# Optimization experiments

Measured on AMD Instinct MI355X. Metric: run time of the kernel, lower is better.

The kernel has to match this reference:

```python
import jax, jax.numpy as jnp
import numpy as np

DIM = 256
DT_REF = 1.0
EPS = 1e-7
GATE_MIN, GATE_MAX = 0.01, 0.99


def _safe_forcing(exp_arg):
    # expm1(z)/z with denominator regularized by sign of real part (matches torch _safe_forcing)
    safe_denom = exp_arg + EPS * jnp.sign(exp_arg.real + EPS)
    return (jnp.exp(exp_arg) - 1.0) / safe_denom


def setup_inputs() -> dict:
    key = jax.random.key(0)
    ks = jax.random.split(key, 12)
    B, T, D = 8, 4096, DIM
    x_mean_seq = jax.random.normal(ks[0], (B, T, D), dtype=jnp.float32)
    dt_seq = jax.random.uniform(ks[1], (B, T), dtype=jnp.float32)
    # GlobalFluxTracker params
    decay_re = jax.random.normal(ks[2], (D,), dtype=jnp.float32) * 0.1 - 1.0
    decay_im = jax.random.normal(ks[3], (D,), dtype=jnp.float32) * 0.1
    W_in = jax.random.normal(ks[4], (2 * D, 2 * D), dtype=jnp.float32) * (1.0 / np.sqrt(2 * D))
    b_in = jnp.zeros((2 * D,), dtype=jnp.float32)
    W_out = jax.random.normal(ks[5], (2 * D, 2 * D), dtype=jnp.float32) * (1.0 / np.sqrt(2 * D))
    b_out = jnp.zeros((2 * D,), dtype=jnp.float32)
    W_gate = jax.random.normal(ks[6], (D, 2 * D), dtype=jnp.float32) * (1.0 / np.sqrt(2 * D))
    b_gate = jnp.zeros((D,), dtype=jnp.float32)
    # TemporalPropagator diagonal generator params
    lam_re = jax.random.normal(ks[7], (D,), dtype=jnp.float32) * 0.01
    lam_im = jax.random.normal(ks[8], (D,), dtype=jnp.float32) * 0.1
    return {
        "x_mean_seq": x_mean_seq, "dt_seq": dt_seq,
        "decay_re": decay_re, "decay_im": decay_im,
        "W_in": W_in, "b_in": b_in, "W_out": W_out, "b_out": b_out,
        "W_gate": W_gate, "b_gate": b_gate,
        "lam_re": lam_re, "lam_im": lam_im,
    }


def reference(x_mean_seq, dt_seq, decay_re, decay_im, W_in, b_in,
              W_out, b_out, W_gate, b_gate, lam_re, lam_im):
    # dt ratio [B,T,1]
    dt_ratio = (dt_seq / DT_REF)[..., None]

    # --- GlobalFluxTracker.get_scan_operators ---
    lam_f = -jax.nn.softplus(decay_re) + 1j * decay_im          # [D] complex64
    exp_arg = lam_f[None, None, :] * dt_ratio                    # [B,T,D]
    decay = jnp.exp(exp_arg)                                     # [B,T,D]
    forcing = _safe_forcing(exp_arg)                             # [B,T,D]

    # _mix_input on real input (imag part is zero)
    x_cat = jnp.concatenate([x_mean_seq, jnp.zeros_like(x_mean_seq)], axis=-1)
    x_in = x_cat @ W_in.T + b_in                                 # [B,T,2D]
    x_re, x_im = jnp.split(x_in, 2, axis=-1)
    x_mixed = x_re + 1j * x_im                                   # [B,T,D]
    X_scan = x_mixed * forcing                                   # [B,T,D]

    # --- linear recurrence flux_t = decay_t * flux_{t-1} + X_t (associative scan over T) ---
    def combine(c1, c2):
        a1, b1 = c1
        a2, b2 = c2
        return (a1 * a2, b1 * a2 + b2)
    _, flux = jax.lax.associative_scan(combine, (decay, X_scan), axis=1)  # [B,T,D]

    # --- compute_output_seq ---
    s_cat = jnp.concatenate([flux.real, flux.imag], axis=-1)     # [B,T,2D]
    src = s_cat @ W_out.T + b_out
    src_re, src_im = jnp.split(src, 2, axis=-1)
    gate = jax.nn.sigmoid(s_cat @ W_gate.T + b_gate)
    gate = gate * (GATE_MAX - GATE_MIN) + GATE_MIN               # [B,T,D]

    # --- TemporalPropagator.get_transition_operators_seq ---
    lam_p = -jax.nn.softplus(lam_re) + 1j * lam_im
    exp_arg_p = lam_p[None, None, :] * dt_ratio
    decay_p = jnp.exp(exp_arg_p)
    forcing_p = _safe_forcing(exp_arg_p)

    out = jnp.concatenate([
        src_re, src_im, gate,
        decay_p.real, decay_p.imag, forcing_p.real, forcing_p.imag,
    ], axis=-1)                                                  # [B,T,7D]
    return out
```

## Files before the change

kernel.cpp:

```cpp
#include <hip/hip_runtime.h>
#include <math.h>

#define DD 256
#define TT 4096
#define NBATCH 8
#define BTOK 32768
#define EPSF 1e-7f

typedef __attribute__((ext_vector_type(4))) float f32x4;
typedef __attribute__((ext_vector_type(8))) short bf16x8;

__device__ __forceinline__ float softplusf(float x) {
  float e = __expf(-fabsf(x));
  return fmaxf(x, 0.f) + __logf(1.f + e);
}
__device__ __forceinline__ float bf2f(unsigned short u) {
  union { unsigned int i; float f; } v; v.i = ((unsigned int)u) << 16; return v.f;
}
__device__ __forceinline__ unsigned short f2bf(float f) {
  union { float f; unsigned int i; } v; v.f = f;
  unsigned int x = v.i;
  unsigned int lsb = (x >> 16) & 1u;
  x += 0x7fffu + lsb;
  return (unsigned short)(x >> 16);
}
__device__ __forceinline__ void decay_forcing(float are, float aim,
    float& dre, float& dim, float& fre, float& fim) {
  float e = __expf(are);
  float s = __sinf(aim), c = __cosf(aim);
  dre = e * c; dim = e * s;
  float sg = (are + EPSF >= 0.f) ? 1.f : -1.f;
  float denr = are + EPSF * sg;
  float deni = aim;
  float inv = __builtin_amdgcn_rcpf(denr * denr + deni * deni);
  float nr = dre - 1.f, ni = dim;
  fre = (nr * denr + ni * deni) * inv;
  fim = (ni * denr - nr * deni) * inv;
}
__device__ __forceinline__ void gl_lds16(const void* g, void* l) {
  __builtin_amdgcn_global_load_lds(
      (const __attribute__((address_space(1))) unsigned int*)g,
      (__attribute__((address_space(3))) unsigned int*)l, 16, 0, 0);
}

__global__ __launch_bounds__(256) void prep(
    const float* __restrict__ x, unsigned short* __restrict__ Xb,
    const float* __restrict__ Win, unsigned short* __restrict__ Wp1)
{
  const int bid = blockIdx.x;
  if (bid < 8192) {
    size_t i = ((size_t)bid * 256 + threadIdx.x) * 4;
    float4 v = *reinterpret_cast<const float4*>(&x[i]);
    ushort4 u;
    u.x = f2bf(v.x); u.y = f2bf(v.y); u.z = f2bf(v.z); u.w = f2bf(v.w);
    *reinterpret_cast<ushort4*>(&Xb[i]) = u;
  } else {
    const int p = bid - 8192;
    const int k = threadIdx.x;
    const int g = p >> 5, r = p & 31;
    const int src = (r < 16) ? (g * 16 + r) : (256 + g * 16 + (r - 16));
    Wp1[(size_t)p * 256 + k] = f2bf(Win[(size_t)src * 512 + k]);
  }
}

__global__ __launch_bounds__(256) void k1_mfma(
    const unsigned short* __restrict__ Xb,
    const unsigned short* __restrict__ Wp,
    const float* __restrict__ bin, const float* __restrict__ dts,
    const float* __restrict__ decr, const float* __restrict__ deci,
    unsigned int* __restrict__ Xri)
{
  __shared__ __align__(16) unsigned short As[128 * 64];
  __shared__ __align__(16) unsigned short Bs[128 * 64];
  const int bx = blockIdx.x;
  const int wg = (bx & 7) * 128 + (bx >> 3);
  const int mt = wg >> 2, nt = wg & 3;
  const int m0 = mt * 128, n0 = nt * 128;
  const int tid = threadIdx.x;
  const int lane = tid & 63, wid = tid >> 6;
  const int wr = wid >> 1, wc = wid & 1;
  const int l15 = lane & 15, hi = lane >> 4;
  const int lrow = tid >> 3;
  const int sslot = (tid & 7) ^ (lrow & 7);
  f32x4 acc[4][4];
  f32x4 z = {0.f, 0.f, 0.f, 0.f};
#pragma unroll
  for (int i = 0; i < 4; ++i)
#pragma unroll
    for (int j = 0; j < 4; ++j) acc[i][j] = z;

  for (int k0 = 0; k0 < 256; k0 += 64) {
    __syncthreads();
#pragma unroll
    for (int c = 0; c < 4; ++c) {
      gl_lds16(&Xb[(size_t)(m0 + c * 32 + lrow) * 256 + k0 + sslot * 8],
               &As[c * 2048 + tid * 8]);
      gl_lds16(&Wp[(size_t)(n0 + c * 32 + lrow) * 256 + k0 + sslot * 8],
               &Bs[c * 2048 + tid * 8]);
    }
    __syncthreads();
#pragma unroll
    for (int kk = 0; kk < 2; ++kk) {
      bf16x8 af[4], bfr[4];
      const int rslot = ((kk * 4 + hi) ^ (l15 & 7)) * 8;
#pragma unroll
      for (int m = 0; m < 4; ++m)
        af[m] = *reinterpret_cast<const bf16x8*>(&As[(wr * 64 + m * 16 + l15) * 64 + rslot]);
#pragma unroll
      for (int n = 0; n < 4; ++n)
        bfr[n] = *reinterpret_cast<const bf16x8*>(&Bs[(wc * 64 + n * 16 + l15) * 64 + rslot]);
#pragma unroll
      for (int m = 0; m < 4; ++m)
#pragma unroll
        for (int n = 0; n < 4; ++n)
          acc[m][n] = __builtin_amdgcn_mfma_f32_16x16x32_bf16(af[m], bfr[n], acc[m][n], 0, 0, 0);
    }
  }

  const int pbase = n0 + wc * 64;
#pragma unroll
  for (int pr = 0; pr < 2; ++pr) {
    const int d = (pbase >> 1) + pr * 16 + l15;
    const float nre = -softplusf(decr[d]);
    const float di = deci[d];
    const float br = bin[d], bi = bin[d + 256];
#pragma unroll
    for (int m = 0; m < 4; ++m) {
#pragma unroll
      for (int r = 0; r < 4; ++r) {
        const int row = m0 + wr * 64 + m * 16 + hi * 4 + r;
        float xr = acc[m][2 * pr][r] + br;
        float xi = acc[m][2 * pr + 1][r] + bi;
        float dt = dts[row];
        float are = nre * dt, aim = di * dt;
        float dr_, dm_, fr_, fm_;
        decay_forcing(are, aim, dr_, dm_, fr_, fm_);
        unsigned int pk = (unsigned int)f2bf(xr * fr_ - xi * fm_)
                        | ((unsigned int)f2bf(xr * fm_ + xi * fr_) << 16);
        Xri[(size_t)row * DD + d] = pk;
      }
    }
  }
}

__global__ __launch_bounds__(256) void k2a_wp3(
    const unsigned int* __restrict__ Xri,
    const float* __restrict__ dts, const float* __restrict__ decr,
    const float* __restrict__ deci,
    float4* __restrict__ ops,
    const float* __restrict__ Wout, const float* __restrict__ Wgate,
    unsigned short* __restrict__ Wp3)
{
  const int bx = blockIdx.x;
  if (bx >= 512) {
    const int p = bx - 512;
    const float* src = (p < 512) ? (Wout + (size_t)p * 512)
                                 : (Wgate + (size_t)(p - 512) * 512);
    Wp3[(size_t)p * 512 + threadIdx.x] = f2bf(src[threadIdx.x]);
    Wp3[(size_t)p * 512 + threadIdx.x + 256] = f2bf(src[threadIdx.x + 256]);
    return;
  }
  const int b = bx >> 6, c = bx & 63;
  const int d = threadIdx.x;
  __shared__ float sdt[64];
  if (threadIdx.x < 64) sdt[threadIdx.x] = dts[b * TT + c * 64 + threadIdx.x];
  const float nre = -softplusf(decr[d]);
  const float di = deci[d];
  __syncthreads();
  float Ar = 1.f, Ai = 0.f, Br = 0.f, Bi = 0.f;
  size_t base = (size_t)(b * TT + c * 64) * DD + d;
  for (int i = 0; i < 64; ++i) {
    float dt = sdt[i];
    float e = __expf(nre * dt);
    float s = __sinf(di * dt), cs = __cosf(di * dt);
    float ar = e * cs, ai = e * s;
    unsigned int pk = Xri[base]; base += DD;
    float xr = bf2f((unsigned short)(pk & 0xffffu));
    float xi = bf2f((unsigned short)(pk >> 16));
    float nAr = Ar * ar - Ai * ai, nAi = Ar * ai + Ai * ar;
    Ar = nAr; Ai = nAi;
    float nBr = Br * ar - Bi * ai + xr, nBi = Br * ai + Bi * ar + xi;
    Br = nBr; Bi = nBi;
  }
  ops[(size_t)bx * DD + d] = make_float4(Ar, Ai, Br, Bi);
}

__global__ __launch_bounds__(256) void k2c_apply(
    const unsigned int* __restrict__ Xri,
    const float* __restrict__ dts, const float* __restrict__ decr,
    const float* __restrict__ deci,
    const float4* __restrict__ ops,
    unsigned short* __restrict__ F)
{
  const int bx = blockIdx.x;
  const int b = bx >> 6, c = bx & 63;
  const int d = threadIdx.x;
  __shared__ float sdt[64];
  if (threadIdx.x < 64) sdt[threadIdx.x] = dts[b * TT + c * 64 + threadIdx.x];
  const float nre = -softplusf(decr[d]);
  const float di = deci[d];
  __syncthreads();

  float hr = 0.f, hi2 = 0.f;
  const size_t obase = (size_t)(b * 64) * DD + d;
  for (int c0 = 0; c0 < c; c0 += 8) {
    float4 oo[8];
#pragma unroll
    for (int j = 0; j < 8; ++j)
      oo[j] = (c0 + j < c) ? ops[obase + (size_t)(c0 + j) * DD]
                           : make_float4(1.f, 0.f, 0.f, 0.f);
#pragma unroll
    for (int j = 0; j < 8; ++j) {
      float nr = oo[j].x * hr - oo[j].y * hi2 + oo[j].z;
      float ni = oo[j].x * hi2 + oo[j].y * hr + oo[j].w;
      hr = nr; hi2 = ni;
    }
  }

  const int tok0 = b * TT + c * 64;
  size_t base = (size_t)tok0 * DD + d;
  for (int i = 0; i < 64; ++i) {
    float dt = sdt[i];
    float e = __expf(nre * dt);
    float s = __sinf(di * dt), cs = __cosf(di * dt);
    float ar = e * cs, ai = e * s;
    unsigned int pk = Xri[base]; base += DD;
    float xr = bf2f((unsigned short)(pk & 0xffffu));
    float xi = bf2f((unsigned short)(pk >> 16));
    float nr = ar * hr - ai * hi2 + xr;
    float ni = ar * hi2 + ai * hr + xi;
    hr = nr; hi2 = ni;
    size_t fb = (size_t)(tok0 + i) * 512 + d;
    F[fb] = f2bf(hr);
    F[fb + 256] = f2bf(hi2);
  }
}

__global__ __launch_bounds__(256) void k3k4(
    const unsigned short* __restrict__ F,
    const unsigned short* __restrict__ Wp,
    const float* __restrict__ bout, const float* __restrict__ bgate,
    const float* __restrict__ dts, const float* __restrict__ lre,
    const float* __restrict__ lim,
    float* __restrict__ out)
{
  __shared__ __align__(16) unsigned short As[128 * 64];
  __shared__ __align__(16) unsigned short Bs[128 * 64];

  const int q = blockIdx.x / 5, r5 = blockIdx.x % 5;

  if (r5 >= 3) {
    const int pb = q * 2 + (r5 - 3);
    const int d = threadIdx.x;
    const float nl = -softplusf(lre[d]);
    const float li = lim[d];
    const int tok0 = pb * 32;
#pragma unroll 4
    for (int i = 0; i < 32; ++i) {
      const int tok = tok0 + i;
      float dt = dts[tok];
      float dr, dm, fr, fm;
      decay_forcing(nl * dt, li * dt, dr, dm, fr, fm);
      float* o = out + (size_t)tok * 1792 + 768;
      __builtin_nontemporal_store(dr, &o[d]);
      __builtin_nontemporal_store(dm, &o[256 + d]);
      __builtin_nontemporal_store(fr, &o[512 + d]);
      __builtin_nontemporal_store(fm, &o[768 + d]);
    }
    return;
  }

  const int gw = q * 3 + r5;
  const int wg = (gw & 7) * 192 + (gw >> 3);
  const int mt = wg / 6, nt = wg % 6;
  const int m0 = mt * 128, n0 = nt * 128;
  const int tid = threadIdx.x;
  const int lane = tid & 63, wid = tid >> 6;
  const int wr = wid >> 1, wc = wid & 1;
  const int l15 = lane & 15, hi = lane >> 4;
  const int lrow = tid >> 3;
  const int sslot = (tid & 7) ^ (lrow & 7);
  f32x4 acc[4][4];
  f32x4 z = {0.f, 0.f, 0.f, 0.f};
#pragma unroll
  for (int i = 0; i < 4; ++i)
#pragma unroll
    for (int j = 0; j < 4; ++j) acc[i][j] = z;

  for (int k0 = 0; k0 < 512; k0 += 64) {
    __syncthreads();
#pragma unroll
    for (int c = 0; c < 4; ++c) {
      gl_lds16(&F[(size_t)(m0 + c * 32 + lrow) * 512 + k0 + sslot * 8],
               &As[c * 2048 + tid * 8]);
      gl_lds16(&Wp[(size_t)(n0 + c * 32 + lrow) * 512 + k0 + sslot * 8],
               &Bs[c * 2048 + tid * 8]);
    }
    __syncthreads();
    __builtin_amdgcn_s_setprio(1);
#pragma unroll
    for (int kk = 0; kk < 2; ++kk) {
      bf16x8 af[4], bfr[4];
      const int rslot = ((kk * 4 + hi) ^ (l15 & 7)) * 8;
#pragma unroll
      for (int m = 0; m < 4; ++m)
        af[m] = *reinterpret_cast<const bf16x8*>(&As[(wr * 64 + m * 16 + l15) * 64 + rslot]);
#pragma unroll
      for (int n = 0; n < 4; ++n)
        bfr[n] = *reinterpret_cast<const bf16x8*>(&Bs[(wc * 64 + n * 16 + l15) * 64 + rslot]);
#pragma unroll
      for (int m = 0; m < 4; ++m)
#pragma unroll
        for (int n = 0; n < 4; ++n)
          acc[m][n] = __builtin_amdgcn_mfma_f32_16x16x32_bf16(af[m], bfr[n], acc[m][n], 0, 0, 0);
    }
    __builtin_amdgcn_s_setprio(0);
  }

  const int nb = n0 + wc * 64;
  if (nb < 512) {
#pragma unroll
    for (int j = 0; j < 4; ++j) {
      const int col = nb + j * 16 + l15;
      const float bb = bout[col];
#pragma unroll
      for (int m = 0; m < 4; ++m)
#pragma unroll
        for (int r = 0; r < 4; ++r) {
          const int row = m0 + wr * 64 + m * 16 + hi * 4 + r;
          __builtin_nontemporal_store(acc[m][j][r] + bb, &out[(size_t)row * 1792 + col]);
        }
    }
  } else {
#pragma unroll
    for (int j = 0; j < 4; ++j) {
      const int col = nb + j * 16 + l15;
      const float bb = bgate[col - 512];
#pragma unroll
      for (int m = 0; m < 4; ++m)
#pragma unroll
        for (int r = 0; r < 4; ++r) {
          const int row = m0 + wr * 64 + m * 16 + hi * 4 + r;
          float g = __builtin_amdgcn_rcpf(1.f + __expf(-(acc[m][j][r] + bb)));
          __builtin_nontemporal_store(g * 0.98f + 0.01f, &out[(size_t)row * 1792 + col]);
        }
    }
  }
}

extern "C" void kernel_launch(void* const* d_in, const int* in_sizes, int n_in,
                              void* d_out, int out_size, void* d_ws, size_t ws_size,
                              hipStream_t stream)
{
  const float* x     = (const float*)d_in[0];
  const float* dts   = (const float*)d_in[1];
  const float* decr  = (const float*)d_in[2];
  const float* deci  = (const float*)d_in[3];
  const float* Win   = (const float*)d_in[4];
  const float* bin   = (const float*)d_in[5];
  const float* Wout  = (const float*)d_in[6];
  const float* bout  = (const float*)d_in[7];
  const float* Wgate = (const float*)d_in[8];
  const float* bgate = (const float*)d_in[9];
  const float* lre   = (const float*)d_in[10];
  const float* lim   = (const float*)d_in[11];
  float* out = (float*)d_out;
  char* ws = (char*)d_ws;

  unsigned short* F   = (unsigned short*)(ws);
  unsigned short* Xb  = (unsigned short*)(ws + (size_t)16 * 1024 * 1024);
  unsigned int*  Xri  = (unsigned int*)(ws + (size_t)32 * 1024 * 1024);
  unsigned short* Wp1 = (unsigned short*)(ws + (size_t)64 * 1024 * 1024);
  unsigned short* Wp3 = (unsigned short*)(ws + (size_t)64 * 1024 * 1024 + 262144);
  float4* ops = (float4*)(ws + (size_t)65 * 1024 * 1024);

  prep<<<8704, 256, 0, stream>>>(x, Xb, Win, Wp1);
  k1_mfma<<<1024, 256, 0, stream>>>(Xb, Wp1, bin, dts, decr, deci, Xri);
  k2a_wp3<<<1280, 256, 0, stream>>>(Xri, dts, decr, deci, ops, Wout, Wgate, Wp3);
  k2c_apply<<<512, 256, 0, stream>>>(Xri, dts, decr, deci, ops, F);
  k3k4<<<2560, 256, 0, stream>>>(F, Wp3, bout, bgate, dts, lre, lim, out);
}
```

Measured before the change: 124.6 us.

## Double-buffer GEMM LDS tiles with K=32 stages and vmcnt-based prefetch

```diff
diff --git a/kernel.cpp b/kernel.cpp
--- a/kernel.cpp
+++ b/kernel.cpp
@@ -244,8 +244,8 @@
     const float* __restrict__ lim,
     float* __restrict__ out)
 {
-  __shared__ __align__(16) unsigned short As[128 * 64];
-  __shared__ __align__(16) unsigned short Bs[128 * 64];
+  __shared__ __align__(16) unsigned short As[2][128 * 32];
+  __shared__ __align__(16) unsigned short Bs[2][128 * 32];
 
   const int q = blockIdx.x / 5, r5 = blockIdx.x % 5;
 
@@ -278,8 +278,22 @@
   const int lane = tid & 63, wid = tid >> 6;
   const int wr = wid >> 1, wc = wid & 1;
   const int l15 = lane & 15, hi = lane >> 4;
-  const int lrow = tid >> 3;
-  const int sslot = (tid & 7) ^ (lrow & 7);
+  const int srow = tid >> 2;
+  const int sq = tid & 3;
+  const int scol = ((sq ^ (srow & 3)) * 8);
+
+#define K3_STAGE(bi, k0)                                                          \
+  {                                                                               \
+    gl_lds16(&F[(size_t)(m0 + srow) * 512 + (k0) + scol],                         \
+             &As[bi][srow * 32 + sq * 8]);                                        \
+    gl_lds16(&F[(size_t)(m0 + 64 + srow) * 512 + (k0) + scol],                    \
+             &As[bi][(64 + srow) * 32 + sq * 8]);                                 \
+    gl_lds16(&Wp[(size_t)(n0 + srow) * 512 + (k0) + scol],                        \
+             &Bs[bi][srow * 32 + sq * 8]);                                        \
+    gl_lds16(&Wp[(size_t)(n0 + 64 + srow) * 512 + (k0) + scol],                   \
+             &Bs[bi][(64 + srow) * 32 + sq * 8]);                                 \
+  }
+
   f32x4 acc[4][4];
   f32x4 z = {0.f, 0.f, 0.f, 0.f};
 #pragma unroll
@@ -287,35 +301,36 @@
 #pragma unroll
     for (int j = 0; j < 4; ++j) acc[i][j] = z;
 
-  for (int k0 = 0; k0 < 512; k0 += 64) {
-    __syncthreads();
-#pragma unroll
-    for (int c = 0; c < 4; ++c) {
-      gl_lds16(&F[(size_t)(m0 + c * 32 + lrow) * 512 + k0 + sslot * 8],
-               &As[c * 2048 + tid * 8]);
-      gl_lds16(&Wp[(size_t)(n0 + c * 32 + lrow) * 512 + k0 + sslot * 8],
-               &Bs[c * 2048 + tid * 8]);
-    }
-    __syncthreads();
+  K3_STAGE(0, 0);
+  K3_STAGE(1, 32);
+
+  const int rq = (hi ^ (l15 & 3)) * 8;
+  for (int step = 0; step < 16; ++step) {
+    const int cur = step & 1;
+    if (step < 15) asm volatile("s_waitcnt vmcnt(4)" ::: "memory");
+    else           asm volatile("s_waitcnt vmcnt(0)" ::: "memory");
+    __builtin_amdgcn_s_barrier();
+    asm volatile("" ::: "memory");
     __builtin_amdgcn_s_setprio(1);
-#pragma unroll
-    for (int kk = 0; kk < 2; ++kk) {
-      bf16x8 af[4], bfr[4];
-      const int rslot = ((kk * 4 + hi) ^ (l15 & 7)) * 8;
-#pragma unroll
-      for (int m = 0; m < 4; ++m)
-        af[m] = *reinterpret_cast<const bf16x8*>(&As[(wr * 64 + m * 16 + l15) * 64 + rslot]);
+    bf16x8 af[4], bfr[4];
+#pragma unroll
+    for (int m = 0; m < 4; ++m)
+      af[m] = *reinterpret_cast<const bf16x8*>(&As[cur][(wr * 64 + m * 16 + l15) * 32 + rq]);
+#pragma unroll
+    for (int n = 0; n < 4; ++n)
+      bfr[n] = *reinterpret_cast<const bf16x8*>(&Bs[cur][(wc * 64 + n * 16 + l15) * 32 + rq]);
+#pragma unroll
+    for (int m = 0; m < 4; ++m)
 #pragma unroll
       for (int n = 0; n < 4; ++n)
-        bfr[n] = *reinterpret_cast<const bf16x8*>(&Bs[(wc * 64 + n * 16 + l15) * 64 + rslot]);
-#pragma unroll
-      for (int m = 0; m < 4; ++m)
-#pragma unroll
-        for (int n = 0; n < 4; ++n)
-          acc[m][n] = __builtin_amdgcn_mfma_f32_16x16x32_bf16(af[m], bfr[n], acc[m][n], 0, 0, 0);
-    }
+        acc[m][n] = __builtin_amdgcn_mfma_f32_16x16x32_bf16(af[m], bfr[n], acc[m][n], 0, 0, 0);
     __builtin_amdgcn_s_setprio(0);
-  }
+    asm volatile("" ::: "memory");
+    __builtin_amdgcn_s_barrier();
+    asm volatile("" ::: "memory");
+    if (step < 14) K3_STAGE(cur, (step + 2) * 32);
+  }
+#undef K3_STAGE
 
   const int nb = n0 + wc * 64;
   if (nb < 512) {
```

Result: no change. 125.9 us (+1.0%).
